# Optimization experiments

Hardware: AMD Instinct MI355X
Metric: run time of the kernel (lower is better)

## Reference

```python
import jax, jax.numpy as jnp
import numpy as np

EPS = 1e-4

def _mlp2(x, W1, b1, W2, b2):
    # Sequential(Linear, ReLU, Linear) -> [*, 1]
    return jax.nn.relu(x @ W1 + b1) @ W2 + b2

def setup_inputs() -> dict:
    N, D = 400, 64
    key = jax.random.key(0)
    ks = jax.random.split(key, 24)
    s = 0.1
    inp = {
        "t": 0,
        "node_edge_embedding": jax.random.normal(ks[0], (N + N * N, D), jnp.float32),
        "node_flow_norm": jax.random.normal(ks[1], (N, D), jnp.float32),
        "A_ne": jax.random.uniform(ks[2], (N, N * N), jnp.float32),
        "node_num": N,
        # alpha_n_dedunce
        "W_alpha": jax.random.normal(ks[3], (D, D), jnp.float32) * s,
        "b_alpha": jnp.zeros((D,), jnp.float32),
        # gamma_e_dedunce
        "W_gamma": jax.random.normal(ks[4], (D, D), jnp.float32) * s,
        "b_gamma": jnp.zeros((D,), jnp.float32),
        # node_to_edge (2D -> D)
        "W_n2e": jax.random.normal(ks[5], (2 * D, D), jnp.float32) * s,
        "b_n2e": jnp.zeros((D,), jnp.float32),
        # edge_to_value: D -> D//2 -> 1
        "W_ev1": jax.random.normal(ks[6], (D, D // 2), jnp.float32) * s,
        "b_ev1": jnp.zeros((D // 2,), jnp.float32),
        "W_ev2": jax.random.normal(ks[7], (D // 2, 1), jnp.float32) * s,
        "b_ev2": jnp.zeros((1,), jnp.float32),
        # f_theta: D -> D//2 -> 1
        "W_ft1": jax.random.normal(ks[8], (D, D // 2), jnp.float32) * s,
        "b_ft1": jnp.zeros((D // 2,), jnp.float32),
        "W_ft2": jax.random.normal(ks[9], (D // 2, 1), jnp.float32) * s,
        "b_ft2": jnp.zeros((1,), jnp.float32),
        # W_3, W_4 (init.normal_ std=0.1)
        "W3": jax.random.normal(ks[10], (D, D), jnp.float32) * s,
        "W4": jax.random.normal(ks[11], (D, D), jnp.float32) * s,
        # edge_to_edge
        "W_e2e": jax.random.normal(ks[12], (D, D), jnp.float32) * s,
        "b_e2e": jnp.zeros((D,), jnp.float32),
        # node_to_edge_2 (2D -> D)
        "W_n2e2": jax.random.normal(ks[13], (2 * D, D), jnp.float32) * s,
        "b_n2e2": jnp.zeros((D,), jnp.float32),
    }
    return inp

def reference(t, node_edge_embedding, node_flow_norm, A_ne, node_num,
              W_alpha, b_alpha, W_gamma, b_gamma, W_n2e, b_n2e,
              W_ev1, b_ev1, W_ev2, b_ev2, W_ft1, b_ft1, W_ft2, b_ft2,
              W3, W4, W_e2e, b_e2e, W_n2e2, b_n2e2):
    N = node_num
    D = node_flow_norm.shape[1]
    node_emb = node_edge_embedding[:N]          # [N, D]
    edge_emb = node_edge_embedding[N:]          # [N*N, D]

    # fully-connected cartesian edge features: edges[i*N+j] = [node_i, node_j]
    edges = jnp.concatenate(
        [jnp.broadcast_to(node_emb[:, None, :], (N, N, D)),
         jnp.broadcast_to(node_emb[None, :, :], (N, N, D))], axis=-1
    ).reshape(N * N, 2 * D)                     # [N*N, 2D]

    h = edges @ W_n2e + b_n2e                   # node_to_edge
    A = jax.nn.relu(_mlp2(h, W_ev1, b_ev1, W_ev2, b_ev2)).reshape(N, N)

    # degree normalization: D_mat A D_mat with D_mat = diag(1/sqrt(clamp(rowsum)))
    d = 1.0 / jnp.sqrt(jnp.maximum(jnp.sum(A, axis=1), EPS))  # [N]
    normalized_A = d[:, None] * A * d[None, :]

    massage_conv = (normalized_A @ node_emb) @ W3
    alpha_n = massage_conv @ W_alpha + b_alpha
    alpha_n = alpha_n / jnp.maximum(jnp.max(jnp.abs(alpha_n)), EPS)

    denominator = _mlp2(node_flow_norm, W_ft1, b_ft1, W_ft2, b_ft2)   # [N,1]
    norm_value = _mlp2(node_emb, W_ft1, b_ft1, W_ft2, b_ft2) / \
        jnp.where(denominator == 0, EPS, denominator)
    node_self_evolve = norm_value * (jax.nn.relu(node_flow_norm - node_emb) @ W4)
    node_self_evolve = alpha_n * node_self_evolve

    gamma_e = jax.nn.softmax(edge_emb @ W_gamma + b_gamma, axis=1)    # [N*N, D]
    edge_indicator = jnp.where(A < 1.0, 0.0, 1.0).reshape(-1, 1)      # [N*N, 1]
    Aggr_edge = A_ne @ (edge_indicator * gamma_e * edge_emb)          # [N, D]
    pred_node = node_self_evolve + Aggr_edge

    edge_self_evolve = edge_emb @ W_e2e + b_e2e
    edge_infonode = edges @ W_n2e2 + b_n2e2
    pred_edge = edge_indicator * (edge_self_evolve + edge_infonode)

    pred_node_edge = jnp.concatenate([pred_node, pred_edge], axis=0)
    return pred_node_edge, edge_indicator
```

## Files before the change

kernel.cpp:

```cpp
#include <hip/hip_runtime.h>

#define NV_N 400
#define NN   160000
#define EPSV 1e-4f
#define IND_BASE ((size_t)160400 * 64)

#define OFF_A    0
#define OFF_P2   160000
#define OFF_Q2   172800
#define OFF_R    185600
#define OFF_S    211200
#define OFF_V4   236800
#define OFF_AR   262400
#define OFF_NV   288000
#define OFF_DV   288400
#define OFF_GMAX 288800
#define OFF_CNT  288832
#define OFF_LIST 289280
#define OFF_WV   449280

__global__ __launch_bounds__(256) void k0_fill_pre(
    const float* __restrict__ NEE, const float* __restrict__ NFN,
    const float* __restrict__ W_n2e, const float* __restrict__ b_n2e,
    const float* __restrict__ W_n2e2, const float* __restrict__ b_n2e2,
    const float* __restrict__ W_ev1, const float* __restrict__ b_ev1,
    const float* __restrict__ W4,
    const float* __restrict__ W_ft1, const float* __restrict__ b_ft1,
    const float* __restrict__ W_ft2, const float* __restrict__ b_ft2,
    float* __restrict__ ws, float* __restrict__ out)
{
    __shared__ float xne[64], xnf[64], tP[64], tQ[64], hidN[32], hidF[32];
    int b = blockIdx.x, t = threadIdx.x;
    if (b < NV_N) {
        int i = b;
        if (t < 64) { xne[t] = NEE[i*64+t]; xnf[t] = NFN[i*64+t]; }
        if (b == 0 && t == 0) ((unsigned*)(ws + OFF_GMAX))[0] = 0u;
        __syncthreads();
        if (t < 64) {
            int dd = t;
            float pv = b_n2e[dd], qv = 0.f, rv = b_n2e2[dd], sv = 0.f, v4 = 0.f;
            for (int k = 0; k < 64; ++k) {
                float xk = xne[k];
                pv += xk * W_n2e[k*64+dd];
                qv += xk * W_n2e[(64+k)*64+dd];
                rv += xk * W_n2e2[k*64+dd];
                sv += xk * W_n2e2[(64+k)*64+dd];
                v4 += fmaxf(xnf[k]-xk, 0.f) * W4[k*64+dd];
            }
            tP[dd] = pv; tQ[dd] = qv;
            ws[OFF_R  + i*64+dd] = rv;
            ws[OFF_S  + i*64+dd] = sv;
            ws[OFF_V4 + i*64+dd] = v4;
        } else if (t >= 64 && t < 96) {
            int dd = t - 64;
            float hn = b_ft1[dd], hf = b_ft1[dd];
            for (int k = 0; k < 64; ++k) { hn += xne[k]*W_ft1[k*32+dd]; hf += xnf[k]*W_ft1[k*32+dd]; }
            hidN[dd] = fmaxf(hn, 0.f); hidF[dd] = fmaxf(hf, 0.f);
        }
        __syncthreads();
        if (t < 32) {
            float p2 = b_ev1[t], q2 = 0.f;
            for (int c = 0; c < 64; ++c) { p2 += tP[c]*W_ev1[c*32+t]; q2 += tQ[c]*W_ev1[c*32+t]; }
            ws[OFF_P2 + i*32+t] = p2;
            ws[OFF_Q2 + i*32+t] = q2;
        }
        if (t == 96) {
            float num = b_ft2[0], den = b_ft2[0];
            for (int c = 0; c < 32; ++c) { num += hidN[c]*W_ft2[c]; den += hidF[c]*W_ft2[c]; }
            float dv = (den == 0.f) ? EPSV : den;
            ws[OFF_NV + i] = num / dv;
        }
    }
    const float4 z4 = make_float4(0.f, 0.f, 0.f, 0.f);
    float4* dst = (float4*)(out + (size_t)NV_N * 64);
    size_t nq = (size_t)NN * 16;
    for (size_t q = (size_t)b*256 + t; q < nq; q += (size_t)gridDim.x * 256)
        dst[q] = z4;
}

__global__ __launch_bounds__(256) void k2_row(
    const float* __restrict__ NEE,
    const float* __restrict__ W_ev2, const float* __restrict__ b_ev2,
    const float* __restrict__ W_e2e, const float* __restrict__ b_e2e,
    float* __restrict__ ws, float* __restrict__ out)
{
    __shared__ float p2s[32], wev2[32], red[256];
    __shared__ int rcnt[256];
    __shared__ unsigned char flag[NV_N];
    __shared__ int act[NV_N];
    __shared__ int s_cnt;
    int i = blockIdx.x, t = threadIdx.x;
    if (t < 32) { p2s[t] = ws[OFF_P2 + i*32+t]; wev2[t] = W_ev2[t]; }
    __syncthreads();
    float b2 = b_ev2[0];
    float s = 0.f; int cc = 0;
    for (int j = t; j < NV_N; j += 256) {
        float v = b2;
        #pragma unroll
        for (int c = 0; c < 32; ++c) {
            float h = p2s[c] + ws[OFF_Q2 + j*32+c];
            v += fmaxf(h, 0.f) * wev2[c];
        }
        float a = fmaxf(v, 0.f);
        ws[OFF_A + i*NV_N + j] = a;
        bool f = (a >= 1.0f);
        flag[j] = f ? 1 : 0;
        out[IND_BASE + (size_t)i*NV_N + j] = f ? 1.f : 0.f;
        s += a; cc += f ? 1 : 0;
    }
    red[t] = s; rcnt[t] = cc;
    __syncthreads();
    for (int st = 128; st > 0; st >>= 1) {
        if (t < st) { red[t] += red[t+st]; rcnt[t] += rcnt[t+st]; }
        __syncthreads();
    }
    if (t == 0) {
        ws[OFF_DV + i] = rsqrtf(fmaxf(red[0], EPSV));
        ((int*)ws)[OFF_CNT + i] = rcnt[0];
    }
    if (t < 64) {
        int base = 0;
        for (int ch = 0; ch < 7; ++ch) {
            int j = ch*64 + t;
            bool f = (j < NV_N) && (flag[j] != 0);
            unsigned long long m = __ballot(f);
            if (f) {
                int pre = __popcll(m & ((1ull << t) - 1ull));
                act[base + pre] = j;
            }
            base += __popcll(m);
        }
        if (t == 0) s_cnt = base;
    }
    __syncthreads();
    int cnt = s_cnt, lane = t & 63, w = t >> 6;
    for (int k = w; k < cnt; k += 4) {
        int j = act[k];
        int e = i*NV_N + j;
        float emb = NEE[(size_t)(NV_N + e)*64 + lane];
        float v = b_e2e[lane] + ws[OFF_R + i*64 + lane] + ws[OFF_S + j*64 + lane];
        #pragma unroll
        for (int c = 0; c < 64; ++c) v += __shfl(emb, c) * W_e2e[c*64 + lane];
        out[(size_t)(NV_N + e)*64 + lane] = v;
    }
}

__global__ __launch_bounds__(256) void k3_alpha_compact(
    const float* __restrict__ NEE,
    const float* __restrict__ W3,
    const float* __restrict__ W_alpha, const float* __restrict__ b_alpha,
    const float* __restrict__ W_gamma, const float* __restrict__ b_gamma,
    float* __restrict__ ws, int cap)
{
    __shared__ float part[4][64];
    __shared__ int red[256];
    __shared__ int s_off;
    int i = blockIdx.x, t = threadIdx.x, lane = t & 63, w = t >> 6;
    int os = 0;
    for (int r = t; r < i; r += 256) os += ((const int*)ws)[OFF_CNT + r];
    red[t] = os; __syncthreads();
    for (int st = 128; st > 0; st >>= 1) { if (t < st) red[t] += red[t+st]; __syncthreads(); }
    if (t == 0) s_off = red[0];
    float acc = 0.f;
    for (int j = w*100; j < w*100 + 100; ++j) {
        float coef = ws[OFF_A + i*NV_N + j] * ws[OFF_DV + j];
        acc += coef * NEE[j*64 + lane];
    }
    part[w][lane] = acc;
    __syncthreads();
    if (w == 0) {
        float nm = (part[0][lane] + part[1][lane] + part[2][lane] + part[3][lane]) * ws[OFF_DV + i];
        float mc = 0.f;
        #pragma unroll
        for (int c = 0; c < 64; ++c) mc += __shfl(nm, c) * W3[c*64 + lane];
        float ar = b_alpha[lane];
        #pragma unroll
        for (int c = 0; c < 64; ++c) ar += __shfl(mc, c) * W_alpha[c*64 + lane];
        ws[OFF_AR + i*64 + lane] = ar;
        float mx = fabsf(ar);
        #pragma unroll
        for (int off = 32; off > 0; off >>= 1) mx = fmaxf(mx, __shfl_xor(mx, off));
        if (lane == 0) atomicMax((unsigned*)(ws + OFF_GMAX), __float_as_uint(mx));
    } else if (w == 1) {
        int base = 0;
        for (int ch = 0; ch < 7; ++ch) {
            int j = ch*64 + lane;
            float a = (j < NV_N) ? ws[OFF_A + i*NV_N + j] : 0.f;
            bool f = (a >= 1.0f);
            unsigned long long m = __ballot(f);
            if (f) {
                int pre = __popcll(m & ((1ull << lane) - 1ull));
                int slot = s_off + base + pre;
                if (slot < cap) ((int*)ws)[OFF_LIST + slot] = i*NV_N + j;
            }
            base += __popcll(m);
        }
    }
    __syncthreads();
    int cnt = ((const int*)ws)[OFF_CNT + i];
    for (int k = w; k < cnt; k += 4) {
        int slot = s_off + k;
        if (slot >= cap) break;
        int e = ((const int*)ws)[OFF_LIST + slot];
        float emb = NEE[(size_t)(NV_N + e)*64 + lane];
        float g = b_gamma[lane];
        #pragma unroll
        for (int c = 0; c < 64; ++c) g += __shfl(emb, c) * W_gamma[c*64 + lane];
        float mx = g;
        #pragma unroll
        for (int off = 32; off > 0; off >>= 1) mx = fmaxf(mx, __shfl_xor(mx, off));
        float p = __expf(g - mx);
        float ssum = p;
        #pragma unroll
        for (int off = 32; off > 0; off >>= 1) ssum += __shfl_xor(ssum, off);
        ws[OFF_WV + (size_t)slot*64 + lane] = (p / ssum) * emb;
    }
}

#define LCHUNK 8192
__global__ __launch_bounds__(256) void k4_final(
    const float* __restrict__ A_ne,
    const float* __restrict__ ws, int cap,
    float* __restrict__ out)
{
    __shared__ float av[LCHUNK];
    __shared__ float part[4][64];
    __shared__ int red[256];
    int i = blockIdx.x, t = threadIdx.x, lane = t & 63, w = t >> 6;
    int os = 0;
    for (int r = t; r < NV_N; r += 256) os += ((const int*)ws)[OFF_CNT + r];
    red[t] = os; __syncthreads();
    for (int st = 128; st > 0; st >>= 1) { if (t < st) red[t] += red[t+st]; __syncthreads(); }
    int nnz = red[0]; if (nnz > cap) nnz = cap;
    const float* Arow = A_ne + (size_t)i * NN;
    float acc = 0.f;
    for (int base = 0; base < nnz; base += LCHUNK) {
        int m = nnz - base; if (m > LCHUNK) m = LCHUNK;
        __syncthreads();
        for (int l = t; l < m; l += 256) {
            int e = ((const int*)ws)[OFF_LIST + base + l];
            av[l] = Arow[e];
        }
        __syncthreads();
        for (int l = w; l < m; l += 4)
            acc = fmaf(av[l], ws[OFF_WV + (size_t)(base + l)*64 + lane], acc);
    }
    part[w][lane] = acc;
    __syncthreads();
    if (w == 0) {
        float aggr = part[0][lane] + part[1][lane] + part[2][lane] + part[3][lane];
        float amax = fmaxf(__uint_as_float(((const unsigned*)(ws + OFF_GMAX))[0]), EPSV);
        float v = (ws[OFF_AR + i*64 + lane] / amax) * ws[OFF_NV + i] * ws[OFF_V4 + i*64 + lane];
        out[i*64 + lane] = v + aggr;
    }
}

extern "C" void kernel_launch(void* const* d_in, const int* in_sizes, int n_in,
                              void* d_out, int out_size, void* d_ws, size_t ws_size,
                              hipStream_t stream) {
    const float* NEE     = (const float*)d_in[1];
    const float* NFN     = (const float*)d_in[2];
    const float* A_ne    = (const float*)d_in[3];
    const float* W_alpha = (const float*)d_in[5];
    const float* b_alpha = (const float*)d_in[6];
    const float* W_gamma = (const float*)d_in[7];
    const float* b_gamma = (const float*)d_in[8];
    const float* W_n2e   = (const float*)d_in[9];
    const float* b_n2e   = (const float*)d_in[10];
    const float* W_ev1   = (const float*)d_in[11];
    const float* b_ev1   = (const float*)d_in[12];
    const float* W_ev2   = (const float*)d_in[13];
    const float* b_ev2   = (const float*)d_in[14];
    const float* W_ft1   = (const float*)d_in[15];
    const float* b_ft1   = (const float*)d_in[16];
    const float* W_ft2   = (const float*)d_in[17];
    const float* b_ft2   = (const float*)d_in[18];
    const float* W3      = (const float*)d_in[19];
    const float* W4      = (const float*)d_in[20];
    const float* W_e2e   = (const float*)d_in[21];
    const float* b_e2e   = (const float*)d_in[22];
    const float* W_n2e2  = (const float*)d_in[23];
    const float* b_n2e2  = (const float*)d_in[24];
    float* out = (float*)d_out;
    float* ws  = (float*)d_ws;

    long long cap_ll = ((long long)(ws_size / 4) - OFF_WV) / 64;
    int cap = (cap_ll > NN) ? NN : (cap_ll < 0 ? 0 : (int)cap_ll);

    hipLaunchKernelGGL(k0_fill_pre, dim3(2048), dim3(256), 0, stream,
        NEE, NFN, W_n2e, b_n2e, W_n2e2, b_n2e2, W_ev1, b_ev1, W4,
        W_ft1, b_ft1, W_ft2, b_ft2, ws, out);
    hipLaunchKernelGGL(k2_row, dim3(NV_N), dim3(256), 0, stream,
        NEE, W_ev2, b_ev2, W_e2e, b_e2e, ws, out);
    hipLaunchKernelGGL(k3_alpha_compact, dim3(NV_N), dim3(256), 0, stream,
        NEE, W3, W_alpha, b_alpha, W_gamma, b_gamma, ws, cap);
    hipLaunchKernelGGL(k4_final, dim3(NV_N), dim3(256), 0, stream,
        A_ne, ws, cap, out);
}
```

Baseline: 41.91 us.

## Fuse row, alpha/compact, and final kernels into one persistent kernel with grid barriers

Merges the three per-row kernels into a single 400-block kernel separated by software grid barriers built on atomic counters and generation flags. The A row, alpha result and active-edge list now stay in shared memory across phases instead of round-tripping through workspace, and the Q2 reads are vectorised to float4. This is meant to remove two kernel launch gaps and some global traffic. In exchange it relies on all 400 blocks being co-resident (the larger shared footprint could limit occupancy), and the spin cap could break the barrier early and give wrong results.

```diff
diff --git a/kernel.cpp b/kernel.cpp
--- a/kernel.cpp
+++ b/kernel.cpp
@@ -5,21 +5,46 @@
 #define EPSV 1e-4f
 #define IND_BASE ((size_t)160400 * 64)
 
-#define OFF_A    0
 #define OFF_P2   160000
 #define OFF_Q2   172800
 #define OFF_R    185600
 #define OFF_S    211200
 #define OFF_V4   236800
-#define OFF_AR   262400
 #define OFF_NV   288000
 #define OFF_DV   288400
 #define OFF_GMAX 288800
+#define BAR_C0   288804
+#define BAR_G0   288812
+#define BAR_C1   288820
+#define BAR_G1   288828
 #define OFF_CNT  288832
 #define OFF_LIST 289280
 #define OFF_WV   449280
 
-__global__ __launch_bounds__(256) void k0_fill_pre(
+#define SPIN_CAP 2000000
+
+__device__ __forceinline__ void grid_bar(unsigned* cnt, unsigned* gen, unsigned nb) {
+    __syncthreads();
+    if (threadIdx.x == 0) {
+        __threadfence();
+        unsigned g = __hip_atomic_load(gen, __ATOMIC_RELAXED, __HIP_MEMORY_SCOPE_AGENT);
+        unsigned old = __hip_atomic_fetch_add(cnt, 1u, __ATOMIC_ACQ_REL, __HIP_MEMORY_SCOPE_AGENT);
+        if (old == nb - 1u) {
+            __hip_atomic_store(cnt, 0u, __ATOMIC_RELAXED, __HIP_MEMORY_SCOPE_AGENT);
+            __hip_atomic_fetch_add(gen, 1u, __ATOMIC_RELEASE, __HIP_MEMORY_SCOPE_AGENT);
+        } else {
+            int spins = 0;
+            while (__hip_atomic_load(gen, __ATOMIC_ACQUIRE, __HIP_MEMORY_SCOPE_AGENT) == g) {
+                __builtin_amdgcn_s_sleep(8);
+                if (++spins > SPIN_CAP) break;
+            }
+        }
+        __threadfence();
+    }
+    __syncthreads();
+}
+
+__global__ __launch_bounds__(256) void kA_fill_pre(
     const float* __restrict__ NEE, const float* __restrict__ NFN,
     const float* __restrict__ W_n2e, const float* __restrict__ b_n2e,
     const float* __restrict__ W_n2e2, const float* __restrict__ b_n2e2,
@@ -34,7 +59,11 @@
     if (b < NV_N) {
         int i = b;
         if (t < 64) { xne[t] = NEE[i*64+t]; xnf[t] = NFN[i*64+t]; }
-        if (b == 0 && t == 0) ((unsigned*)(ws + OFF_GMAX))[0] = 0u;
+        if (b == 0 && t == 0) {
+            __hip_atomic_store((unsigned*)ws + OFF_GMAX, 0u, __ATOMIC_RELAXED, __HIP_MEMORY_SCOPE_AGENT);
+            __hip_atomic_store((unsigned*)ws + BAR_C0, 0u, __ATOMIC_RELAXED, __HIP_MEMORY_SCOPE_AGENT);
+            __hip_atomic_store((unsigned*)ws + BAR_C1, 0u, __ATOMIC_RELAXED, __HIP_MEMORY_SCOPE_AGENT);
+        }
         __syncthreads();
         if (t < 64) {
             int dd = t;
@@ -78,180 +107,172 @@
         dst[q] = z4;
 }
 
-__global__ __launch_bounds__(256) void k2_row(
+#define LCHUNK 4096
+__global__ __launch_bounds__(256) void kB_fused(
     const float* __restrict__ NEE,
+    const float* __restrict__ A_ne,
     const float* __restrict__ W_ev2, const float* __restrict__ b_ev2,
     const float* __restrict__ W_e2e, const float* __restrict__ b_e2e,
-    float* __restrict__ ws, float* __restrict__ out)
-{
-    __shared__ float p2s[32], wev2[32], red[256];
-    __shared__ int rcnt[256];
-    __shared__ unsigned char flag[NV_N];
-    __shared__ int act[NV_N];
-    __shared__ int s_cnt;
-    int i = blockIdx.x, t = threadIdx.x;
-    if (t < 32) { p2s[t] = ws[OFF_P2 + i*32+t]; wev2[t] = W_ev2[t]; }
-    __syncthreads();
-    float b2 = b_ev2[0];
-    float s = 0.f; int cc = 0;
-    for (int j = t; j < NV_N; j += 256) {
-        float v = b2;
-        #pragma unroll
-        for (int c = 0; c < 32; ++c) {
-            float h = p2s[c] + ws[OFF_Q2 + j*32+c];
-            v += fmaxf(h, 0.f) * wev2[c];
-        }
-        float a = fmaxf(v, 0.f);
-        ws[OFF_A + i*NV_N + j] = a;
-        bool f = (a >= 1.0f);
-        flag[j] = f ? 1 : 0;
-        out[IND_BASE + (size_t)i*NV_N + j] = f ? 1.f : 0.f;
-        s += a; cc += f ? 1 : 0;
-    }
-    red[t] = s; rcnt[t] = cc;
-    __syncthreads();
-    for (int st = 128; st > 0; st >>= 1) {
-        if (t < st) { red[t] += red[t+st]; rcnt[t] += rcnt[t+st]; }
-        __syncthreads();
-    }
-    if (t == 0) {
-        ws[OFF_DV + i] = rsqrtf(fmaxf(red[0], EPSV));
-        ((int*)ws)[OFF_CNT + i] = rcnt[0];
-    }
-    if (t < 64) {
-        int base = 0;
-        for (int ch = 0; ch < 7; ++ch) {
-            int j = ch*64 + t;
-            bool f = (j < NV_N) && (flag[j] != 0);
-            unsigned long long m = __ballot(f);
-            if (f) {
-                int pre = __popcll(m & ((1ull << t) - 1ull));
-                act[base + pre] = j;
-            }
-            base += __popcll(m);
-        }
-        if (t == 0) s_cnt = base;
-    }
-    __syncthreads();
-    int cnt = s_cnt, lane = t & 63, w = t >> 6;
-    for (int k = w; k < cnt; k += 4) {
-        int j = act[k];
-        int e = i*NV_N + j;
-        float emb = NEE[(size_t)(NV_N + e)*64 + lane];
-        float v = b_e2e[lane] + ws[OFF_R + i*64 + lane] + ws[OFF_S + j*64 + lane];
-        #pragma unroll
-        for (int c = 0; c < 64; ++c) v += __shfl(emb, c) * W_e2e[c*64 + lane];
-        out[(size_t)(NV_N + e)*64 + lane] = v;
-    }
-}
-
-__global__ __launch_bounds__(256) void k3_alpha_compact(
-    const float* __restrict__ NEE,
     const float* __restrict__ W3,
     const float* __restrict__ W_alpha, const float* __restrict__ b_alpha,
     const float* __restrict__ W_gamma, const float* __restrict__ b_gamma,
-    float* __restrict__ ws, int cap)
+    float* ws, int cap, float* __restrict__ out)
 {
+    __shared__ float p2s[32], wev2[32], redf[256];
+    __shared__ int redi[256];
+    __shared__ float arow[NV_N];
+    __shared__ int act[NV_N];
+    __shared__ float s_ar[64];
     __shared__ float part[4][64];
-    __shared__ int red[256];
-    __shared__ int s_off;
+    __shared__ float av[LCHUNK];
+    __shared__ int s_cnt, s_off;
     int i = blockIdx.x, t = threadIdx.x, lane = t & 63, w = t >> 6;
-    int os = 0;
-    for (int r = t; r < i; r += 256) os += ((const int*)ws)[OFF_CNT + r];
-    red[t] = os; __syncthreads();
-    for (int st = 128; st > 0; st >>= 1) { if (t < st) red[t] += red[t+st]; __syncthreads(); }
-    if (t == 0) s_off = red[0];
-    float acc = 0.f;
-    for (int j = w*100; j < w*100 + 100; ++j) {
-        float coef = ws[OFF_A + i*NV_N + j] * ws[OFF_DV + j];
-        acc += coef * NEE[j*64 + lane];
-    }
-    part[w][lane] = acc;
+    unsigned nb = gridDim.x;
+
+    if (t < 32) { p2s[t] = ws[OFF_P2 + i*32+t]; wev2[t] = W_ev2[t]; }
     __syncthreads();
-    if (w == 0) {
-        float nm = (part[0][lane] + part[1][lane] + part[2][lane] + part[3][lane]) * ws[OFF_DV + i];
-        float mc = 0.f;
-        #pragma unroll
-        for (int c = 0; c < 64; ++c) mc += __shfl(nm, c) * W3[c*64 + lane];
-        float ar = b_alpha[lane];
-        #pragma unroll
-        for (int c = 0; c < 64; ++c) ar += __shfl(mc, c) * W_alpha[c*64 + lane];
-        ws[OFF_AR + i*64 + lane] = ar;
-        float mx = fabsf(ar);
-        #pragma unroll
-        for (int off = 32; off > 0; off >>= 1) mx = fmaxf(mx, __shfl_xor(mx, off));
-        if (lane == 0) atomicMax((unsigned*)(ws + OFF_GMAX), __float_as_uint(mx));
-    } else if (w == 1) {
-        int base = 0;
-        for (int ch = 0; ch < 7; ++ch) {
-            int j = ch*64 + lane;
-            float a = (j < NV_N) ? ws[OFF_A + i*NV_N + j] : 0.f;
+    {
+        float b2 = b_ev2[0];
+        float s = 0.f; int cc = 0;
+        for (int j = t; j < NV_N; j += 256) {
+            const float4* q2row = (const float4*)&ws[OFF_Q2 + j*32];
+            float v = b2;
+            #pragma unroll
+            for (int c4 = 0; c4 < 8; ++c4) {
+                float4 q = q2row[c4];
+                v += fmaxf(p2s[c4*4+0]+q.x, 0.f) * wev2[c4*4+0];
+                v += fmaxf(p2s[c4*4+1]+q.y, 0.f) * wev2[c4*4+1];
+                v += fmaxf(p2s[c4*4+2]+q.z, 0.f) * wev2[c4*4+2];
+                v += fmaxf(p2s[c4*4+3]+q.w, 0.f) * wev2[c4*4+3];
+            }
+            float a = fmaxf(v, 0.f);
+            arow[j] = a;
             bool f = (a >= 1.0f);
-            unsigned long long m = __ballot(f);
-            if (f) {
-                int pre = __popcll(m & ((1ull << lane) - 1ull));
-                int slot = s_off + base + pre;
-                if (slot < cap) ((int*)ws)[OFF_LIST + slot] = i*NV_N + j;
-            }
-            base += __popcll(m);
-        }
-    }
-    __syncthreads();
-    int cnt = ((const int*)ws)[OFF_CNT + i];
-    for (int k = w; k < cnt; k += 4) {
-        int slot = s_off + k;
-        if (slot >= cap) break;
-        int e = ((const int*)ws)[OFF_LIST + slot];
-        float emb = NEE[(size_t)(NV_N + e)*64 + lane];
-        float g = b_gamma[lane];
-        #pragma unroll
-        for (int c = 0; c < 64; ++c) g += __shfl(emb, c) * W_gamma[c*64 + lane];
-        float mx = g;
-        #pragma unroll
-        for (int off = 32; off > 0; off >>= 1) mx = fmaxf(mx, __shfl_xor(mx, off));
-        float p = __expf(g - mx);
-        float ssum = p;
-        #pragma unroll
-        for (int off = 32; off > 0; off >>= 1) ssum += __shfl_xor(ssum, off);
-        ws[OFF_WV + (size_t)slot*64 + lane] = (p / ssum) * emb;
-    }
-}
-
-#define LCHUNK 8192
-__global__ __launch_bounds__(256) void k4_final(
-    const float* __restrict__ A_ne,
-    const float* __restrict__ ws, int cap,
-    float* __restrict__ out)
-{
-    __shared__ float av[LCHUNK];
-    __shared__ float part[4][64];
-    __shared__ int red[256];
-    int i = blockIdx.x, t = threadIdx.x, lane = t & 63, w = t >> 6;
-    int os = 0;
-    for (int r = t; r < NV_N; r += 256) os += ((const int*)ws)[OFF_CNT + r];
-    red[t] = os; __syncthreads();
-    for (int st = 128; st > 0; st >>= 1) { if (t < st) red[t] += red[t+st]; __syncthreads(); }
-    int nnz = red[0]; if (nnz > cap) nnz = cap;
-    const float* Arow = A_ne + (size_t)i * NN;
-    float acc = 0.f;
-    for (int base = 0; base < nnz; base += LCHUNK) {
-        int m = nnz - base; if (m > LCHUNK) m = LCHUNK;
-        __syncthreads();
-        for (int l = t; l < m; l += 256) {
-            int e = ((const int*)ws)[OFF_LIST + base + l];
-            av[l] = Arow[e];
-        }
-        __syncthreads();
-        for (int l = w; l < m; l += 4)
-            acc = fmaf(av[l], ws[OFF_WV + (size_t)(base + l)*64 + lane], acc);
-    }
-    part[w][lane] = acc;
-    __syncthreads();
-    if (w == 0) {
-        float aggr = part[0][lane] + part[1][lane] + part[2][lane] + part[3][lane];
-        float amax = fmaxf(__uint_as_float(((const unsigned*)(ws + OFF_GMAX))[0]), EPSV);
-        float v = (ws[OFF_AR + i*64 + lane] / amax) * ws[OFF_NV + i] * ws[OFF_V4 + i*64 + lane];
-        out[i*64 + lane] = v + aggr;
+            out[IND_BASE + (size_t)i*NV_N + j] = f ? 1.f : 0.f;
+            s += a; cc += f ? 1 : 0;
+        }
+        redf[t] = s; redi[t] = cc;
+        __syncthreads();
+        for (int st = 128; st > 0; st >>= 1) {
+            if (t < st) { redf[t] += redf[t+st]; redi[t] += redi[t+st]; }
+            __syncthreads();
+        }
+        if (t == 0) {
+            ws[OFF_DV + i] = rsqrtf(fmaxf(redf[0], EPSV));
+            ((int*)ws)[OFF_CNT + i] = redi[0];
+        }
+        if (t < 64) {
+            int base = 0;
+            for (int ch = 0; ch < 7; ++ch) {
+                int j = ch*64 + t;
+                bool f = (j < NV_N) && (arow[j] >= 1.0f);
+                unsigned long long m = __ballot(f);
+                if (f) {
+                    int pre = __popcll(m & ((1ull << t) - 1ull));
+                    act[base + pre] = j;
+                }
+                base += __popcll(m);
+            }
+            if (t == 0) s_cnt = base;
+        }
+        __syncthreads();
+        int cnt = s_cnt;
+        for (int k = w; k < cnt; k += 4) {
+            int j = act[k];
+            int e = i*NV_N + j;
+            float emb = NEE[(size_t)(NV_N + e)*64 + lane];
+            float v = b_e2e[lane] + ws[OFF_R + i*64 + lane] + ws[OFF_S + j*64 + lane];
+            #pragma unroll
+            for (int c = 0; c < 64; ++c) v += __shfl(emb, c) * W_e2e[c*64 + lane];
+            out[(size_t)(NV_N + e)*64 + lane] = v;
+        }
+    }
+
+    grid_bar((unsigned*)ws + BAR_C0, (unsigned*)ws + BAR_G0, nb);
+
+    {
+        int os = 0;
+        for (int r = t; r < i; r += 256) os += ((int*)ws)[OFF_CNT + r];
+        redi[t] = os; __syncthreads();
+        for (int st = 128; st > 0; st >>= 1) { if (t < st) redi[t] += redi[t+st]; __syncthreads(); }
+        if (t == 0) s_off = redi[0];
+        for (int j = t; j < NV_N; j += 256) arow[j] *= ws[OFF_DV + j];
+        __syncthreads();
+        float acc = 0.f;
+        for (int j = w*100; j < w*100 + 100; ++j)
+            acc += arow[j] * NEE[j*64 + lane];
+        part[w][lane] = acc;
+        __syncthreads();
+        if (w == 0) {
+            float nm = (part[0][lane] + part[1][lane] + part[2][lane] + part[3][lane]) * ws[OFF_DV + i];
+            float mc = 0.f;
+            #pragma unroll
+            for (int c = 0; c < 64; ++c) mc += __shfl(nm, c) * W3[c*64 + lane];
+            float ar = b_alpha[lane];
+            #pragma unroll
+            for (int c = 0; c < 64; ++c) ar += __shfl(mc, c) * W_alpha[c*64 + lane];
+            s_ar[lane] = ar;
+            float mx = fabsf(ar);
+            #pragma unroll
+            for (int off = 32; off > 0; off >>= 1) mx = fmaxf(mx, __shfl_xor(mx, off));
+            if (lane == 0) atomicMax((unsigned*)ws + OFF_GMAX, __float_as_uint(mx));
+        } else if (w == 1) {
+            for (int k = lane; k < s_cnt; k += 64) {
+                int slot = s_off + k;
+                if (slot < cap) ((int*)ws)[OFF_LIST + slot] = i*NV_N + act[k];
+            }
+        }
+        __syncthreads();
+        int cnt = s_cnt;
+        for (int k = w; k < cnt; k += 4) {
+            int slot = s_off + k;
+            if (slot >= cap) break;
+            int e = i*NV_N + act[k];
+            float emb = NEE[(size_t)(NV_N + e)*64 + lane];
+            float g = b_gamma[lane];
+            #pragma unroll
+            for (int c = 0; c < 64; ++c) g += __shfl(emb, c) * W_gamma[c*64 + lane];
+            float mx = g;
+            #pragma unroll
+            for (int off = 32; off > 0; off >>= 1) mx = fmaxf(mx, __shfl_xor(mx, off));
+            float p = __expf(g - mx);
+            float ssum = p;
+            #pragma unroll
+            for (int off = 32; off > 0; off >>= 1) ssum += __shfl_xor(ssum, off);
+            ws[OFF_WV + (size_t)slot*64 + lane] = (p / ssum) * emb;
+        }
+    }
+
+    grid_bar((unsigned*)ws + BAR_C1, (unsigned*)ws + BAR_G1, nb);
+
+    {
+        int os = 0;
+        for (int r = t; r < NV_N; r += 256) os += ((int*)ws)[OFF_CNT + r];
+        redi[t] = os; __syncthreads();
+        for (int st = 128; st > 0; st >>= 1) { if (t < st) redi[t] += redi[t+st]; __syncthreads(); }
+        int nnz = redi[0]; if (nnz > cap) nnz = cap;
+        const float* Arow = A_ne + (size_t)i * NN;
+        float acc = 0.f;
+        for (int base = 0; base < nnz; base += LCHUNK) {
+            int m = nnz - base; if (m > LCHUNK) m = LCHUNK;
+            __syncthreads();
+            for (int l = t; l < m; l += 256) {
+                int e = ((int*)ws)[OFF_LIST + base + l];
+                av[l] = Arow[e];
+            }
+            __syncthreads();
+            for (int l = w; l < m; l += 4)
+                acc = fmaf(av[l], ws[OFF_WV + (size_t)(base + l)*64 + lane], acc);
+        }
+        part[w][lane] = acc;
+        __syncthreads();
+        if (w == 0) {
+            float aggr = part[0][lane] + part[1][lane] + part[2][lane] + part[3][lane];
+            unsigned gm = __hip_atomic_load((unsigned*)ws + OFF_GMAX, __ATOMIC_RELAXED, __HIP_MEMORY_SCOPE_AGENT);
+            float amax = fmaxf(__uint_as_float(gm), EPSV);
+            float v = (s_ar[lane] / amax) * ws[OFF_NV + i] * ws[OFF_V4 + i*64 + lane];
+            out[i*64 + lane] = v + aggr;
+        }
     }
 }
 
@@ -287,13 +308,10 @@
     long long cap_ll = ((long long)(ws_size / 4) - OFF_WV) / 64;
     int cap = (cap_ll > NN) ? NN : (cap_ll < 0 ? 0 : (int)cap_ll);
 
-    hipLaunchKernelGGL(k0_fill_pre, dim3(2048), dim3(256), 0, stream,
+    hipLaunchKernelGGL(kA_fill_pre, dim3(2048), dim3(256), 0, stream,
         NEE, NFN, W_n2e, b_n2e, W_n2e2, b_n2e2, W_ev1, b_ev1, W4,
         W_ft1, b_ft1, W_ft2, b_ft2, ws, out);
-    hipLaunchKernelGGL(k2_row, dim3(NV_N), dim3(256), 0, stream,
-        NEE, W_ev2, b_ev2, W_e2e, b_e2e, ws, out);
-    hipLaunchKernelGGL(k3_alpha_compact, dim3(NV_N), dim3(256), 0, stream,
-        NEE, W3, W_alpha, b_alpha, W_gamma, b_gamma, ws, cap);
-    hipLaunchKernelGGL(k4_final, dim3(NV_N), dim3(256), 0, stream,
-        A_ne, ws, cap, out);
+    hipLaunchKernelGGL(kB_fused, dim3(NV_N), dim3(256), 0, stream,
+        NEE, A_ne, W_ev2, b_ev2, W_e2e, b_e2e, W3, W_alpha, b_alpha,
+        W_gamma, b_gamma, ws, cap, out);
 }
```

New measurement: 142.9 us. +241.0%, slower.

## Zero only inactive edge rows in row kernel instead of full output prefill

Applied to the files above, without the earlier changes.

Removes the full 41 MB zero-fill of the edge output from the pre-kernel, shrinks that kernel to one block per node, and instead has each row block in k2_row write zeros only for edges whose indicator is off. Active rows are written once by the edge projection, so the double write for those rows disappears. It also vectorises the Q2 reads with float4 and halves the LDS chunk in k4_final, which may improve occupancy. In exchange, the zero stores now sit on the critical path of k2_row rather than in a separate wide-grid kernel.

```diff
diff --git a/kernel.cpp b/kernel.cpp
--- a/kernel.cpp
+++ b/kernel.cpp
@@ -19,7 +19,7 @@
 #define OFF_LIST 289280
 #define OFF_WV   449280
 
-__global__ __launch_bounds__(256) void k0_fill_pre(
+__global__ __launch_bounds__(256) void kA_pre(
     const float* __restrict__ NEE, const float* __restrict__ NFN,
     const float* __restrict__ W_n2e, const float* __restrict__ b_n2e,
     const float* __restrict__ W_n2e2, const float* __restrict__ b_n2e2,
@@ -27,55 +27,47 @@
     const float* __restrict__ W4,
     const float* __restrict__ W_ft1, const float* __restrict__ b_ft1,
     const float* __restrict__ W_ft2, const float* __restrict__ b_ft2,
-    float* __restrict__ ws, float* __restrict__ out)
+    float* __restrict__ ws)
 {
     __shared__ float xne[64], xnf[64], tP[64], tQ[64], hidN[32], hidF[32];
-    int b = blockIdx.x, t = threadIdx.x;
-    if (b < NV_N) {
-        int i = b;
-        if (t < 64) { xne[t] = NEE[i*64+t]; xnf[t] = NFN[i*64+t]; }
-        if (b == 0 && t == 0) ((unsigned*)(ws + OFF_GMAX))[0] = 0u;
-        __syncthreads();
-        if (t < 64) {
-            int dd = t;
-            float pv = b_n2e[dd], qv = 0.f, rv = b_n2e2[dd], sv = 0.f, v4 = 0.f;
-            for (int k = 0; k < 64; ++k) {
-                float xk = xne[k];
-                pv += xk * W_n2e[k*64+dd];
-                qv += xk * W_n2e[(64+k)*64+dd];
-                rv += xk * W_n2e2[k*64+dd];
-                sv += xk * W_n2e2[(64+k)*64+dd];
-                v4 += fmaxf(xnf[k]-xk, 0.f) * W4[k*64+dd];
-            }
-            tP[dd] = pv; tQ[dd] = qv;
-            ws[OFF_R  + i*64+dd] = rv;
-            ws[OFF_S  + i*64+dd] = sv;
-            ws[OFF_V4 + i*64+dd] = v4;
-        } else if (t >= 64 && t < 96) {
-            int dd = t - 64;
-            float hn = b_ft1[dd], hf = b_ft1[dd];
-            for (int k = 0; k < 64; ++k) { hn += xne[k]*W_ft1[k*32+dd]; hf += xnf[k]*W_ft1[k*32+dd]; }
-            hidN[dd] = fmaxf(hn, 0.f); hidF[dd] = fmaxf(hf, 0.f);
-        }
-        __syncthreads();
-        if (t < 32) {
-            float p2 = b_ev1[t], q2 = 0.f;
-            for (int c = 0; c < 64; ++c) { p2 += tP[c]*W_ev1[c*32+t]; q2 += tQ[c]*W_ev1[c*32+t]; }
-            ws[OFF_P2 + i*32+t] = p2;
-            ws[OFF_Q2 + i*32+t] = q2;
-        }
-        if (t == 96) {
-            float num = b_ft2[0], den = b_ft2[0];
-            for (int c = 0; c < 32; ++c) { num += hidN[c]*W_ft2[c]; den += hidF[c]*W_ft2[c]; }
-            float dv = (den == 0.f) ? EPSV : den;
-            ws[OFF_NV + i] = num / dv;
-        }
-    }
-    const float4 z4 = make_float4(0.f, 0.f, 0.f, 0.f);
-    float4* dst = (float4*)(out + (size_t)NV_N * 64);
-    size_t nq = (size_t)NN * 16;
-    for (size_t q = (size_t)b*256 + t; q < nq; q += (size_t)gridDim.x * 256)
-        dst[q] = z4;
+    int i = blockIdx.x, t = threadIdx.x;
+    if (t < 64) { xne[t] = NEE[i*64+t]; xnf[t] = NFN[i*64+t]; }
+    if (i == 0 && t == 0) ((unsigned*)ws)[OFF_GMAX] = 0u;
+    __syncthreads();
+    if (t < 64) {
+        int dd = t;
+        float pv = b_n2e[dd], qv = 0.f, rv = b_n2e2[dd], sv = 0.f, v4 = 0.f;
+        for (int k = 0; k < 64; ++k) {
+            float xk = xne[k];
+            pv += xk * W_n2e[k*64+dd];
+            qv += xk * W_n2e[(64+k)*64+dd];
+            rv += xk * W_n2e2[k*64+dd];
+            sv += xk * W_n2e2[(64+k)*64+dd];
+            v4 += fmaxf(xnf[k]-xk, 0.f) * W4[k*64+dd];
+        }
+        tP[dd] = pv; tQ[dd] = qv;
+        ws[OFF_R  + i*64+dd] = rv;
+        ws[OFF_S  + i*64+dd] = sv;
+        ws[OFF_V4 + i*64+dd] = v4;
+    } else if (t >= 64 && t < 96) {
+        int dd = t - 64;
+        float hn = b_ft1[dd], hf = b_ft1[dd];
+        for (int k = 0; k < 64; ++k) { hn += xne[k]*W_ft1[k*32+dd]; hf += xnf[k]*W_ft1[k*32+dd]; }
+        hidN[dd] = fmaxf(hn, 0.f); hidF[dd] = fmaxf(hf, 0.f);
+    }
+    __syncthreads();
+    if (t < 32) {
+        float p2 = b_ev1[t], q2 = 0.f;
+        for (int c = 0; c < 64; ++c) { p2 += tP[c]*W_ev1[c*32+t]; q2 += tQ[c]*W_ev1[c*32+t]; }
+        ws[OFF_P2 + i*32+t] = p2;
+        ws[OFF_Q2 + i*32+t] = q2;
+    }
+    if (t == 96) {
+        float num = b_ft2[0], den = b_ft2[0];
+        for (int c = 0; c < 32; ++c) { num += hidN[c]*W_ft2[c]; den += hidF[c]*W_ft2[c]; }
+        float dv = (den == 0.f) ? EPSV : den;
+        ws[OFF_NV + i] = num / dv;
+    }
 }
 
 __global__ __launch_bounds__(256) void k2_row(
@@ -84,7 +76,7 @@
     const float* __restrict__ W_e2e, const float* __restrict__ b_e2e,
     float* __restrict__ ws, float* __restrict__ out)
 {
-    __shared__ float p2s[32], wev2[32], red[256];
+    __shared__ float p2s[32], wev2[32], redf[256];
     __shared__ int rcnt[256];
     __shared__ unsigned char flag[NV_N];
     __shared__ int act[NV_N];
@@ -95,11 +87,15 @@
     float b2 = b_ev2[0];
     float s = 0.f; int cc = 0;
     for (int j = t; j < NV_N; j += 256) {
+        const float4* q2row = (const float4*)&ws[OFF_Q2 + j*32];
         float v = b2;
         #pragma unroll
-        for (int c = 0; c < 32; ++c) {
-            float h = p2s[c] + ws[OFF_Q2 + j*32+c];
-            v += fmaxf(h, 0.f) * wev2[c];
+        for (int c4 = 0; c4 < 8; ++c4) {
+            float4 q = q2row[c4];
+            v += fmaxf(p2s[c4*4+0]+q.x, 0.f) * wev2[c4*4+0];
+            v += fmaxf(p2s[c4*4+1]+q.y, 0.f) * wev2[c4*4+1];
+            v += fmaxf(p2s[c4*4+2]+q.z, 0.f) * wev2[c4*4+2];
+            v += fmaxf(p2s[c4*4+3]+q.w, 0.f) * wev2[c4*4+3];
         }
         float a = fmaxf(v, 0.f);
         ws[OFF_A + i*NV_N + j] = a;
@@ -108,14 +104,14 @@
         out[IND_BASE + (size_t)i*NV_N + j] = f ? 1.f : 0.f;
         s += a; cc += f ? 1 : 0;
     }
-    red[t] = s; rcnt[t] = cc;
+    redf[t] = s; rcnt[t] = cc;
     __syncthreads();
     for (int st = 128; st > 0; st >>= 1) {
-        if (t < st) { red[t] += red[t+st]; rcnt[t] += rcnt[t+st]; }
+        if (t < st) { redf[t] += redf[t+st]; rcnt[t] += rcnt[t+st]; }
         __syncthreads();
     }
     if (t == 0) {
-        ws[OFF_DV + i] = rsqrtf(fmaxf(red[0], EPSV));
+        ws[OFF_DV + i] = rsqrtf(fmaxf(redf[0], EPSV));
         ((int*)ws)[OFF_CNT + i] = rcnt[0];
     }
     if (t < 64) {
@@ -133,6 +129,13 @@
         if (t == 0) s_cnt = base;
     }
     __syncthreads();
+    {
+        const float4 z4 = make_float4(0.f, 0.f, 0.f, 0.f);
+        float4* orow = (float4*)(out + (NV_N + (size_t)i*NV_N) * 64);
+        for (int q = t; q < NV_N*16; q += 256) {
+            if (!flag[q >> 4]) orow[q] = z4;
+        }
+    }
     int cnt = s_cnt, lane = t & 63, w = t >> 6;
     for (int k = w; k < cnt; k += 4) {
         int j = act[k];
@@ -180,7 +183,7 @@
         float mx = fabsf(ar);
         #pragma unroll
         for (int off = 32; off > 0; off >>= 1) mx = fmaxf(mx, __shfl_xor(mx, off));
-        if (lane == 0) atomicMax((unsigned*)(ws + OFF_GMAX), __float_as_uint(mx));
+        if (lane == 0) atomicMax((unsigned*)ws + OFF_GMAX, __float_as_uint(mx));
     } else if (w == 1) {
         int base = 0;
         for (int ch = 0; ch < 7; ++ch) {
@@ -217,7 +220,7 @@
     }
 }
 
-#define LCHUNK 8192
+#define LCHUNK 4096
 __global__ __launch_bounds__(256) void k4_final(
     const float* __restrict__ A_ne,
     const float* __restrict__ ws, int cap,
@@ -249,7 +252,7 @@
     __syncthreads();
     if (w == 0) {
         float aggr = part[0][lane] + part[1][lane] + part[2][lane] + part[3][lane];
-        float amax = fmaxf(__uint_as_float(((const unsigned*)(ws + OFF_GMAX))[0]), EPSV);
+        float amax = fmaxf(__uint_as_float(((const unsigned*)ws)[OFF_GMAX]), EPSV);
         float v = (ws[OFF_AR + i*64 + lane] / amax) * ws[OFF_NV + i] * ws[OFF_V4 + i*64 + lane];
         out[i*64 + lane] = v + aggr;
     }
@@ -287,9 +290,9 @@
     long long cap_ll = ((long long)(ws_size / 4) - OFF_WV) / 64;
     int cap = (cap_ll > NN) ? NN : (cap_ll < 0 ? 0 : (int)cap_ll);
 
-    hipLaunchKernelGGL(k0_fill_pre, dim3(2048), dim3(256), 0, stream,
+    hipLaunchKernelGGL(kA_pre, dim3(NV_N), dim3(256), 0, stream,
         NEE, NFN, W_n2e, b_n2e, W_n2e2, b_n2e2, W_ev1, b_ev1, W4,
-        W_ft1, b_ft1, W_ft2, b_ft2, ws, out);
+        W_ft1, b_ft1, W_ft2, b_ft2, ws);
     hipLaunchKernelGGL(k2_row, dim3(NV_N), dim3(256), 0, stream,
         NEE, W_ev2, b_ev2, W_e2e, b_e2e, ws, out);
     hipLaunchKernelGGL(k3_alpha_compact, dim3(NV_N), dim3(256), 0, stream,
```

Measured after the change: 42.89 us. 2.3% more time.
